# Kernel optimization log

Measured on AMD Instinct MI355X. Metric: run time of the kernel, lower is better.

Reference implementation:

```python
import jax, jax.numpy as jnp
import numpy as np

B, S, K, H, W = 64, 100, 4, 32, 32

def setup_inputs() -> dict:
    key = jax.random.key(0)
    k1, k2 = jax.random.split(key)
    output = jax.random.normal(k1, (B, S, K, H, W), dtype=jnp.float32)
    convdata = jax.random.normal(k2, (B, S, K, H, W), dtype=jnp.float32)
    return {"output": output, "convdata": convdata}

def reference(output, convdata):
    # Original: sum over 32x32 of mean(|convdata[:,:,3,i,j] - output[:,:,3,i,j]|) / 1024
    # Each (i,j) slice has identical size, so this equals a single mean of the
    # abs-diff over the whole [B, S, 32, 32] slice at channel 3.
    return jnp.mean(jnp.abs(convdata[:, :, 3] - output[:, :, 3]))
```

## Files before the change

### kernel.cpp

```cpp
#include <hip/hip_runtime.h>


#define RBLOCKS 2048
#define RTHREADS 256
#define NCHUNKS 6400

__global__ __launch_bounds__(RTHREADS)
void absdiff_partial_kernel(const float4* __restrict__ outp,
                            const float4* __restrict__ conv,
                            float* __restrict__ partials) {
    const int t = threadIdx.x;
    float acc0 = 0.0f, acc1 = 0.0f;

    int c = blockIdx.x;
    for (; c + RBLOCKS < NCHUNKS; c += 2 * RBLOCKS) {
        const size_t g0 = (size_t)c * 1024 + 768 + t;
        const size_t g1 = (size_t)(c + RBLOCKS) * 1024 + 768 + t;
        const float4 a0 = outp[g0];
        const float4 b0 = conv[g0];
        const float4 a1 = outp[g1];
        const float4 b1 = conv[g1];
        acc0 += fabsf(b0.x - a0.x) + fabsf(b0.y - a0.y)
              + fabsf(b0.z - a0.z) + fabsf(b0.w - a0.w);
        acc1 += fabsf(b1.x - a1.x) + fabsf(b1.y - a1.y)
              + fabsf(b1.z - a1.z) + fabsf(b1.w - a1.w);
    }
    if (c < NCHUNKS) {
        const size_t g = (size_t)c * 1024 + 768 + t;
        const float4 a = outp[g];
        const float4 b = conv[g];
        acc0 += fabsf(b.x - a.x) + fabsf(b.y - a.y)
              + fabsf(b.z - a.z) + fabsf(b.w - a.w);
    }
    float acc = acc0 + acc1;

    #pragma unroll
    for (int off = 32; off > 0; off >>= 1)
        acc += __shfl_down(acc, off, 64);

    __shared__ float smem[RTHREADS / 64];
    const int lane = t & 63;
    const int wave = t >> 6;
    if (lane == 0) smem[wave] = acc;
    __syncthreads();
    if (t == 0) {
        float s = 0.0f;
        #pragma unroll
        for (int w = 0; w < RTHREADS / 64; ++w) s += smem[w];
        partials[blockIdx.x] = s;
    }
}

__global__ __launch_bounds__(RTHREADS)
void final_reduce_kernel(const float* __restrict__ partials,
                         float* __restrict__ out, float inv_total) {
    float acc = 0.0f;
    #pragma unroll
    for (int i = 0; i < RBLOCKS / RTHREADS; ++i)
        acc += partials[threadIdx.x + i * RTHREADS];
    #pragma unroll
    for (int off = 32; off > 0; off >>= 1)
        acc += __shfl_down(acc, off, 64);
    __shared__ float smem[RTHREADS / 64];
    const int lane = threadIdx.x & 63;
    const int wave = threadIdx.x >> 6;
    if (lane == 0) smem[wave] = acc;
    __syncthreads();
    if (threadIdx.x == 0) {
        float s = 0.0f;
        #pragma unroll
        for (int w = 0; w < RTHREADS / 64; ++w) s += smem[w];
        out[0] = s * inv_total;
    }
}

extern "C" void kernel_launch(void* const* d_in, const int* in_sizes, int n_in,
                              void* d_out, int out_size, void* d_ws, size_t ws_size,
                              hipStream_t stream) {
    const float4* outp = (const float4*)d_in[0];
    const float4* conv = (const float4*)d_in[1];
    float* partials = (float*)d_ws;
    float* out = (float*)d_out;

    const float inv_total = 1.0f / (float)(64 * 100 * 1024);

    absdiff_partial_kernel<<<RBLOCKS, RTHREADS, 0, stream>>>(outp, conv, partials);
    final_reduce_kernel<<<1, RTHREADS, 0, stream>>>(partials, out, inv_total);
}
```

Before: 180.7 us.

## Fuse final reduction into partial kernel via cooperative grid sync

Replaces the two-kernel reduction with a single cooperative launch that syncs the whole grid and lets block 0 reduce the partials. The grid is halved to 1024 blocks so all blocks can be co-resident, with each block covering more chunks. This removes the second kernel launch and its gap, but adds the cost of a grid-wide barrier and of cooperative launch setup, and the smaller grid may lower memory parallelism.

```diff
diff --git a/kernel.cpp b/kernel.cpp
--- a/kernel.cpp
+++ b/kernel.cpp
@@ -1,14 +1,19 @@
 #include <hip/hip_runtime.h>
+#include <hip/hip_cooperative_groups.h>
+
+namespace cg = cooperative_groups;
 
 
-#define RBLOCKS 2048
+#define RBLOCKS 1024
 #define RTHREADS 256
 #define NCHUNKS 6400
 
 __global__ __launch_bounds__(RTHREADS)
-void absdiff_partial_kernel(const float4* __restrict__ outp,
-                            const float4* __restrict__ conv,
-                            float* __restrict__ partials) {
+void absdiff_coop_kernel(const float4* __restrict__ outp,
+                         const float4* __restrict__ conv,
+                         float* __restrict__ partials,
+                         float* __restrict__ out,
+                         float inv_total) {
     const int t = threadIdx.x;
     float acc0 = 0.0f, acc1 = 0.0f;
 
@@ -49,28 +54,23 @@
         for (int w = 0; w < RTHREADS / 64; ++w) s += smem[w];
         partials[blockIdx.x] = s;
     }
-}
 
-__global__ __launch_bounds__(RTHREADS)
-void final_reduce_kernel(const float* __restrict__ partials,
-                         float* __restrict__ out, float inv_total) {
-    float acc = 0.0f;
-    #pragma unroll
-    for (int i = 0; i < RBLOCKS / RTHREADS; ++i)
-        acc += partials[threadIdx.x + i * RTHREADS];
-    #pragma unroll
-    for (int off = 32; off > 0; off >>= 1)
-        acc += __shfl_down(acc, off, 64);
-    __shared__ float smem[RTHREADS / 64];
-    const int lane = threadIdx.x & 63;
-    const int wave = threadIdx.x >> 6;
-    if (lane == 0) smem[wave] = acc;
-    __syncthreads();
-    if (threadIdx.x == 0) {
-        float s = 0.0f;
+    cg::this_grid().sync();
+
+    if (blockIdx.x == 0) {
+        float a = partials[t] + partials[t + 256]
+                + partials[t + 512] + partials[t + 768];
         #pragma unroll
-        for (int w = 0; w < RTHREADS / 64; ++w) s += smem[w];
-        out[0] = s * inv_total;
+        for (int off = 32; off > 0; off >>= 1)
+            a += __shfl_down(a, off, 64);
+        if (lane == 0) smem[wave] = a;
+        __syncthreads();
+        if (t == 0) {
+            float s = 0.0f;
+            #pragma unroll
+            for (int w = 0; w < RTHREADS / 64; ++w) s += smem[w];
+            out[0] = s * inv_total;
+        }
     }
 }
 
@@ -81,9 +81,11 @@
     const float4* conv = (const float4*)d_in[1];
     float* partials = (float*)d_ws;
     float* out = (float*)d_out;
+    float inv_total = 1.0f / (float)(64 * 100 * 1024);
 
-    const float inv_total = 1.0f / (float)(64 * 100 * 1024);
-
-    absdiff_partial_kernel<<<RBLOCKS, RTHREADS, 0, stream>>>(outp, conv, partials);
-    final_reduce_kernel<<<1, RTHREADS, 0, stream>>>(partials, out, inv_total);
+    void* args[] = {(void*)&outp, (void*)&conv, (void*)&partials,
+                    (void*)&out, (void*)&inv_total};
+    hipLaunchCooperativeKernel((const void*)absdiff_coop_kernel,
+                               dim3(RBLOCKS), dim3(RTHREADS),
+                               args, 0, stream);
 }
```

After: 272.8 us. +51.0%, slower.
